# Kernel optimization log

Measured on AMD Instinct MI355X. Metric: run time of the kernel, lower is better.

Reference implementation:

```python
import jax, jax.numpy as jnp
import numpy as np
from jax import lax

B, T, D = 4, 4096, 1024
H, d = 4, 64
EPS = 1e-6

def pos_unit(x):
    # positive feature map (elu+1) normalized to unit L2 norm along feature dim
    p = jax.nn.elu(x) + 1.0
    return p / (jnp.linalg.norm(p, axis=-1, keepdims=True) + EPS)

def setup_inputs() -> dict:
    key = jax.random.key(0)
    ks = jax.random.split(key, 5)
    s_in = 1.0 / np.sqrt(D)
    s_hd = 1.0 / np.sqrt(H * d)
    return {
        "x": jax.random.normal(ks[0], (B, T, D), dtype=jnp.float32),
        "Wq": jax.random.normal(ks[1], (H * d, D), dtype=jnp.float32) * s_in,
        "Wk": jax.random.normal(ks[2], (H * d, D), dtype=jnp.float32) * s_in,
        "Wv": jax.random.normal(ks[3], (H * d, D), dtype=jnp.float32) * s_in,
        "Wo": jax.random.normal(ks[4], (D, H * d), dtype=jnp.float32) * s_hd,
    }

def reference(x, Wq, Wk, Wv, Wo):
    Bx, Tx, Dx = x.shape
    q = (x @ Wq.T).reshape(Bx, Tx, H, d)
    k = (x @ Wk.T).reshape(Bx, Tx, H, d)
    v = (x @ Wv.T).reshape(Bx, Tx, H, d)
    q = pos_unit(q)
    k = pos_unit(k)
    # time-major for scan: [T, B, H, d]
    qT = jnp.transpose(q, (1, 0, 2, 3))
    kT = jnp.transpose(k, (1, 0, 2, 3))
    vT = jnp.transpose(v, (1, 0, 2, 3))
    kv0 = jnp.zeros((Bx, H, d, d), dtype=x.dtype)  # [B,H,j,d]
    kc0 = jnp.zeros((Bx, H, d), dtype=x.dtype)

    def step(carry, inp):
        kv_cum, k_cum = carry
        qt, kt, vt = inp  # each [B,H,d]
        kv_cum = kv_cum + jnp.einsum('bhd,bhj->bhjd', kt, vt)
        k_cum = k_cum + kt
        num = jnp.einsum('bhd,bhjd->bhj', qt, kv_cum)
        den = jnp.einsum('bhd,bhd->bh', qt, k_cum)[..., None] + EPS
        return (kv_cum, k_cum), num / den

    (kv_f, kc_f), yT = lax.scan(step, (kv0, kc0), (qT, kT, vT))
    y = jnp.transpose(yT, (1, 0, 2, 3)).reshape(Bx, Tx, H * d)
    y = y @ Wo.T
    return y, kv_f, kc_f
```

## Files before the change

### kernel.cpp

```cpp
#include <hip/hip_runtime.h>
#include <hip/hip_bf16.h>
#include <math.h>

#define T_SEQ   4096
#define NB      4
#define NH      4
#define DH      64
#define DM      1024
#define MR      16384
#define NQKV    768
#define CH      64
#define NCH     64
#define SST     4160
#define BHN     16

typedef __attribute__((ext_vector_type(4))) float          f32x4;
typedef __attribute__((ext_vector_type(8))) short          s16x8;
typedef __attribute__((ext_vector_type(4))) unsigned short u16x4;

__device__ __forceinline__ float bf2f(unsigned short u) {
  union { unsigned int i; float f; } c; c.i = ((unsigned int)u) << 16; return c.f;
}
__device__ __forceinline__ unsigned short f2bf(float f) {
  union { float f; unsigned int i; } c; c.f = f;
  unsigned int i = c.i;
  return (unsigned short)((i + 0x7fffu + ((i >> 16) & 1u)) >> 16);
}
__device__ __forceinline__ s16x8 pack8(f32x4 lo, f32x4 hi) {
  s16x8 r;
  r[0] = (short)f2bf(lo.x); r[1] = (short)f2bf(lo.y);
  r[2] = (short)f2bf(lo.z); r[3] = (short)f2bf(lo.w);
  r[4] = (short)f2bf(hi.x); r[5] = (short)f2bf(hi.y);
  r[6] = (short)f2bf(hi.z); r[7] = (short)f2bf(hi.w);
  return r;
}

__global__ __launch_bounds__(256, 2) void gemm_qkv_kernel(
    const float* __restrict__ X,
    const float* __restrict__ Wq,
    const float* __restrict__ Wk,
    const float* __restrict__ Wv,
    unsigned short* __restrict__ C)
{
  constexpr int K = DM;
  constexpr int N = NQKV;
  __shared__ unsigned short sA[128 * 32];
  __shared__ unsigned short sB[128 * 32];

  const int tid  = threadIdx.x;
  const int wave = tid >> 6;
  const int lane = tid & 63;
  const int quad = lane >> 4;
  const int l16  = lane & 15;
  const int wm = (wave >> 1) * 64;
  const int wn = (wave & 1) * 64;

  const int row0 = blockIdx.x * 128;
  const int bn   = blockIdx.y;
  const float* Bt = (bn < 2) ? Wq : (bn < 4) ? Wk : Wv;
  const int brow0 = (bn & 1) * 128;

  const int srow = tid >> 2;
  const int scol = ((tid & 3) ^ (srow & 3)) * 8;
  const float* Ag = X  + (size_t)(row0  + srow) * K + scol;
  const float* Bg = Bt + (size_t)(brow0 + srow) * K + scol;
  unsigned short* sAp = sA + tid * 8;
  unsigned short* sBp = sB + tid * 8;

  const int ra = (quad ^ (l16 & 3)) * 8;

  f32x4 acc[4][4];
  #pragma unroll
  for (int i = 0; i < 4; i++)
    #pragma unroll
    for (int j = 0; j < 4; j++) acc[i][j] = (f32x4){0.f, 0.f, 0.f, 0.f};

  for (int kt = 0; kt < K; kt += 32) {
    const f32x4 a0l = *(const f32x4*)(Ag + kt);
    const f32x4 a0h = *(const f32x4*)(Ag + kt + 4);
    const f32x4 a1l = *(const f32x4*)(Ag + kt + (size_t)64 * K);
    const f32x4 a1h = *(const f32x4*)(Ag + kt + (size_t)64 * K + 4);
    const f32x4 b0l = *(const f32x4*)(Bg + kt);
    const f32x4 b0h = *(const f32x4*)(Bg + kt + 4);
    const f32x4 b1l = *(const f32x4*)(Bg + kt + (size_t)64 * K);
    const f32x4 b1h = *(const f32x4*)(Bg + kt + (size_t)64 * K + 4);
    __syncthreads();
    *(s16x8*)sAp          = pack8(a0l, a0h);
    *(s16x8*)(sAp + 2048) = pack8(a1l, a1h);
    *(s16x8*)sBp          = pack8(b0l, b0h);
    *(s16x8*)(sBp + 2048) = pack8(b1l, b1h);
    __syncthreads();
    s16x8 af[4], bw[4];
    #pragma unroll
    for (int i = 0; i < 4; i++)
      af[i] = *(const s16x8*)(sA + (wm + i * 16 + l16) * 32 + ra);
    #pragma unroll
    for (int j = 0; j < 4; j++)
      bw[j] = *(const s16x8*)(sB + (wn + j * 16 + l16) * 32 + ra);
    #pragma unroll
    for (int i = 0; i < 4; i++)
      #pragma unroll
      for (int j = 0; j < 4; j++)
        acc[i][j] = __builtin_amdgcn_mfma_f32_16x16x32_bf16(af[i], bw[j], acc[i][j], 0, 0, 0);
  }

  const int colb = bn * 128 + wn;
  #pragma unroll
  for (int i = 0; i < 4; i++) {
    const int r = row0 + wm + i * 16 + quad * 4;
    #pragma unroll
    for (int j = 0; j < 4; j++) {
      const int cc = colb + j * 16 + l16;
      #pragma unroll
      for (int g = 0; g < 4; g++)
        C[(size_t)(r + g) * N + cc] = f2bf(acc[i][j][g]);
    }
  }
}

__global__ __launch_bounds__(256, 2) void gemm_out_kernel(
    const unsigned short* __restrict__ Y,
    const float* __restrict__ Wo,
    float* __restrict__ Out)
{
  constexpr int K = 256;
  constexpr int N = DM;
  __shared__ unsigned short sA[128 * 32];
  __shared__ unsigned short sB[128 * 32];

  const int tid  = threadIdx.x;
  const int wave = tid >> 6;
  const int lane = tid & 63;
  const int quad = lane >> 4;
  const int l16  = lane & 15;
  const int wm = (wave >> 1) * 64;
  const int wn = (wave & 1) * 64;

  const int row0  = blockIdx.x * 128;
  const int bcol0 = blockIdx.y * 128;

  const int srow = tid >> 2;
  const int scol = ((tid & 3) ^ (srow & 3)) * 8;
  const unsigned short* Ag = Y  + (size_t)(row0  + srow) * K + scol;
  const float*          Bg = Wo + (size_t)(bcol0 + srow) * K + scol;
  unsigned short* sAp = sA + tid * 8;
  unsigned short* sBp = sB + tid * 8;

  const int ra = (quad ^ (l16 & 3)) * 8;

  f32x4 acc[4][4];
  #pragma unroll
  for (int i = 0; i < 4; i++)
    #pragma unroll
    for (int j = 0; j < 4; j++) acc[i][j] = (f32x4){0.f, 0.f, 0.f, 0.f};

  for (int kt = 0; kt < K; kt += 32) {
    const s16x8 a0 = *(const s16x8*)(Ag + kt);
    const s16x8 a1 = *(const s16x8*)(Ag + kt + (size_t)64 * K);
    const f32x4 b0l = *(const f32x4*)(Bg + kt);
    const f32x4 b0h = *(const f32x4*)(Bg + kt + 4);
    const f32x4 b1l = *(const f32x4*)(Bg + kt + (size_t)64 * K);
    const f32x4 b1h = *(const f32x4*)(Bg + kt + (size_t)64 * K + 4);
    __syncthreads();
    *(s16x8*)sAp          = a0;
    *(s16x8*)(sAp + 2048) = a1;
    *(s16x8*)sBp          = pack8(b0l, b0h);
    *(s16x8*)(sBp + 2048) = pack8(b1l, b1h);
    __syncthreads();
    s16x8 af[4], bw[4];
    #pragma unroll
    for (int i = 0; i < 4; i++)
      af[i] = *(const s16x8*)(sA + (wm + i * 16 + l16) * 32 + ra);
    #pragma unroll
    for (int j = 0; j < 4; j++)
      bw[j] = *(const s16x8*)(sB + (wn + j * 16 + l16) * 32 + ra);
    #pragma unroll
    for (int i = 0; i < 4; i++)
      #pragma unroll
      for (int j = 0; j < 4; j++)
        acc[i][j] = __builtin_amdgcn_mfma_f32_16x16x32_bf16(af[i], bw[j], acc[i][j], 0, 0, 0);
  }

  #pragma unroll
  for (int i = 0; i < 4; i++) {
    const int r = row0 + wm + i * 16 + quad * 4;
    #pragma unroll
    for (int j = 0; j < 4; j++) {
      const int cc = bcol0 + wn + j * 16 + l16;
      #pragma unroll
      for (int g = 0; g < 4; g++)
        Out[(size_t)(r + g) * N + cc] = acc[i][j][g];
    }
  }
}

__global__ __launch_bounds__(256) void chunk_sums_kernel(
    const unsigned short* __restrict__ qkv,
    float* __restrict__ cs)
{
  const int blk = blockIdx.x;
  const int bh = blk >> 6, c = blk & 63;
  const int b = bh >> 2, h = bh & 3;
  __shared__ float sK[CH * DH];
  __shared__ float sV[CH * DH];
  const int wave = threadIdx.x >> 6, lane = threadIdx.x & 63;
  const size_t rowbase = ((size_t)b * T_SEQ + (size_t)c * CH) * NQKV + h * DH;

  #pragma unroll 4
  for (int tt = 0; tt < 16; tt++) {
    const int t = tt * 4 + wave;
    const unsigned short* r = qkv + rowbase + (size_t)t * NQKV;
    const float kx = bf2f(r[256 + lane]);
    const float vx = bf2f(r[512 + lane]);
    float pk = kx > 0.f ? kx + 1.f : __expf(kx);
    float sk = pk * pk;
    #pragma unroll
    for (int o = 32; o > 0; o >>= 1) sk += __shfl_xor(sk, o, 64);
    sK[t * DH + lane] = pk / (sqrtf(sk) + 1e-6f);
    sV[t * DH + lane] = vx;
  }
  __syncthreads();

  const int dg = threadIdx.x >> 4;
  const int jg = threadIdx.x & 15;
  f32x4 a0 = (f32x4){0,0,0,0}, a1 = a0, a2 = a0, a3 = a0;
  for (int t = 0; t < CH; t++) {
    const f32x4 k4 = ((const f32x4*)sK)[t * 16 + dg];
    const f32x4 v4 = ((const f32x4*)sV)[t * 16 + jg];
    a0 += k4.x * v4; a1 += k4.y * v4; a2 += k4.z * v4; a3 += k4.w * v4;
  }
  float* o = cs + (size_t)blk * SST;
  ((f32x4*)(o + (dg * 4 + 0) * 64))[jg] = a0;
  ((f32x4*)(o + (dg * 4 + 1) * 64))[jg] = a1;
  ((f32x4*)(o + (dg * 4 + 2) * 64))[jg] = a2;
  ((f32x4*)(o + (dg * 4 + 3) * 64))[jg] = a3;
  if (threadIdx.x < 64) {
    float s = 0.f;
    for (int t = 0; t < CH; t++) s += sK[t * DH + threadIdx.x];
    o[4096 + threadIdx.x] = s;
  }
}

__global__ __launch_bounds__(256) void scan_kernel(
    float* __restrict__ cs, float* __restrict__ outTail)
{
  const int gid = blockIdx.x * 256 + threadIdx.x;
  const int bh = gid / SST;
  const int e  = gid - bh * SST;
  float run = 0.f;
  size_t idx = (size_t)bh * NCH * SST + e;
  for (int c = 0; c < NCH; c++, idx += SST) {
    const float v = cs[idx];
    cs[idx] = run;
    run += v;
  }
  if (e < 4096) {
    const int dd = e >> 6, j = e & 63;
    outTail[(size_t)bh * 4096 + j * 64 + dd] = run;
  } else {
    const int dd = e - 4096;
    outTail[BHN * 4096 + (size_t)bh * 64 + dd] = run;
  }
}

__global__ __launch_bounds__(256, 4) void chunk_out_kernel(
    const unsigned short* __restrict__ qkv,
    const float* __restrict__ st,
    unsigned short* __restrict__ yatt)
{
  const int blk = blockIdx.x;
  const int bh = blk >> 6;
  const int c  = blk & 63;
  const int b = bh >> 2, h = bh & 3;

  __shared__ __align__(16) unsigned short sQ [64 * 64];
  __shared__ __align__(16) unsigned short sKA[64 * 64];
  __shared__ __align__(16) unsigned short sVt[64 * 64];
  __shared__ __align__(16) unsigned short sSt[64 * 64];
  __shared__ float sKc[64];
  __shared__ float sDen[64];

  const int tid  = threadIdx.x;
  const int wave = tid >> 6, lane = tid & 63;
  const int quad = lane >> 4, l16 = lane & 15;
  const size_t rowbase = ((size_t)b * T_SEQ + (size_t)c * CH) * NQKV + h * DH;

  #pragma unroll 4
  for (int tt = 0; tt < 16; tt++) {
    const int t = tt * 4 + wave;
    const unsigned short* r = qkv + rowbase + (size_t)t * NQKV;
    const float qx = bf2f(r[lane]);
    const float kx = bf2f(r[256 + lane]);
    const unsigned short vu = r[512 + lane];
    float pq = qx > 0.f ? qx + 1.f : __expf(qx);
    float pk = kx > 0.f ? kx + 1.f : __expf(kx);
    float sq = pq * pq, sk = pk * pk;
    #pragma unroll
    for (int o = 32; o > 0; o >>= 1) {
      sq += __shfl_xor(sq, o, 64);
      sk += __shfl_xor(sk, o, 64);
    }
    const int sw = (t & 7) << 3;
    sQ [t * 64 + (lane ^ sw)] = f2bf(pq / (sqrtf(sq) + 1e-6f));
    sKA[t * 64 + (lane ^ sw)] = f2bf(pk / (sqrtf(sk) + 1e-6f));
    sVt[lane * 64 + (t ^ ((lane & 7) << 3))] = vu;
  }
  const float* stp = st + (size_t)blk * SST;
  for (int i = tid; i < 1024; i += 256) {
    const f32x4 s4 = ((const f32x4*)stp)[i];
    const int d = i >> 4, j0 = (i & 15) << 2;
    #pragma unroll
    for (int g = 0; g < 4; g++) {
      const int j = j0 + g;
      sSt[j * 64 + (d ^ ((j & 7) << 3))] = f2bf(s4[g]);
    }
  }
  if (tid < 64) sKc[tid] = stp[4096 + tid];
  __syncthreads();

  const int wr = (wave >> 1) * 32;
  const int wc = (wave & 1) * 32;

  f32x4 accA[2][2];
  #pragma unroll
  for (int i = 0; i < 2; i++)
    #pragma unroll
    for (int j = 0; j < 2; j++) accA[i][j] = (f32x4){0.f, 0.f, 0.f, 0.f};

  #pragma unroll
  for (int ks = 0; ks < 2; ks++) {
    const int grp = ks * 4 + quad;
    s16x8 aq[2], bk[2];
    #pragma unroll
    for (int i = 0; i < 2; i++) {
      const int rq = wr + i * 16 + l16;
      aq[i] = *(const s16x8*)(sQ + rq * 64 + ((grp ^ (rq & 7)) << 3));
    }
    #pragma unroll
    for (int j = 0; j < 2; j++) {
      const int rk = wc + j * 16 + l16;
      bk[j] = *(const s16x8*)(sKA + rk * 64 + ((grp ^ (rk & 7)) << 3));
    }
    #pragma unroll
    for (int i = 0; i < 2; i++)
      #pragma unroll
      for (int j = 0; j < 2; j++)
        accA[i][j] = __builtin_amdgcn_mfma_f32_16x16x32_bf16(aq[i], bk[j], accA[i][j], 0, 0, 0);
  }
  __syncthreads();

  #pragma unroll
  for (int i = 0; i < 2; i++)
    #pragma unroll
    for (int j = 0; j < 2; j++)
      #pragma unroll
      for (int g = 0; g < 4; g++) {
        const int t = wr + i * 16 + quad * 4 + g;
        const int s = wc + j * 16 + l16;
        const float av = (s <= t) ? accA[i][j][g] : 0.f;
        sKA[t * 64 + (s ^ ((t & 7) << 3))] = f2bf(av);
      }
  __syncthreads();

  {
    const int t = tid >> 2, p = tid & 3;
    const int sw = (t & 7) << 3;
    float s = 0.f;
    #pragma unroll
    for (int e = 0; e < 16; e++) {
      const int d = p * 16 + e;
      s += bf2f(sKA[t * 64 + d]);
      s += bf2f(sQ[t * 64 + (d ^ sw)]) * sKc[d];
    }
    s += __shfl_xor(s, 1, 64);
    s += __shfl_xor(s, 2, 64);
    if (p == 0) sDen[t] = s + 1e-6f;
  }
  __syncthreads();

  f32x4 acc[2][2];
  #pragma unroll
  for (int i = 0; i < 2; i++)
    #pragma unroll
    for (int j = 0; j < 2; j++) acc[i][j] = (f32x4){0.f, 0.f, 0.f, 0.f};

  #pragma unroll
  for (int ks = 0; ks < 2; ks++) {
    const int grp = ks * 4 + quad;
    s16x8 aq[2], bs[2];
    #pragma unroll
    for (int i = 0; i < 2; i++) {
      const int rq = wr + i * 16 + l16;
      aq[i] = *(const s16x8*)(sQ + rq * 64 + ((grp ^ (rq & 7)) << 3));
    }
    #pragma unroll
    for (int j = 0; j < 2; j++) {
      const int rj = wc + j * 16 + l16;
      bs[j] = *(const s16x8*)(sSt + rj * 64 + ((grp ^ (rj & 7)) << 3));
    }
    #pragma unroll
    for (int i = 0; i < 2; i++)
      #pragma unroll
      for (int j = 0; j < 2; j++)
        acc[i][j] = __builtin_amdgcn_mfma_f32_16x16x32_bf16(aq[i], bs[j], acc[i][j], 0, 0, 0);
  }
  #pragma unroll
  for (int ks = 0; ks < 2; ks++) {
    const int grp = ks * 4 + quad;
    s16x8 aa[2], bv[2];
    #pragma unroll
    for (int i = 0; i < 2; i++) {
      const int rt = wr + i * 16 + l16;
      aa[i] = *(const s16x8*)(sKA + rt * 64 + ((grp ^ (rt & 7)) << 3));
    }
    #pragma unroll
    for (int j = 0; j < 2; j++) {
      const int rj = wc + j * 16 + l16;
      bv[j] = *(const s16x8*)(sVt + rj * 64 + ((grp ^ (rj & 7)) << 3));
    }
    #pragma unroll
    for (int i = 0; i < 2; i++)
      #pragma unroll
      for (int j = 0; j < 2; j++)
        acc[i][j] = __builtin_amdgcn_mfma_f32_16x16x32_bf16(aa[i], bv[j], acc[i][j], 0, 0, 0);
  }

  #pragma unroll
  for (int i = 0; i < 2; i++)
    #pragma unroll
    for (int g = 0; g < 4; g++) {
      const int t = wr + i * 16 + quad * 4 + g;
      const float inv = 1.f / sDen[t];
      #pragma unroll
      for (int j = 0; j < 2; j++) {
        const int jj = wc + j * 16 + l16;
        const size_t o = ((size_t)b * T_SEQ + (size_t)c * CH + t) * 256 + h * 64 + jj;
        yatt[o] = f2bf(acc[i][j][g] * inv);
      }
    }
}

extern "C" void kernel_launch(void* const* d_in, const int* in_sizes, int n_in,
                              void* d_out, int out_size, void* d_ws, size_t ws_size,
                              hipStream_t stream) {
  const float* X  = (const float*)d_in[0];
  const float* Wq = (const float*)d_in[1];
  const float* Wk = (const float*)d_in[2];
  const float* Wv = (const float*)d_in[3];
  const float* Wo = (const float*)d_in[4];
  float* out = (float*)d_out;

  unsigned short* qkvb = (unsigned short*)d_out;
  float* outTail = out + 16777216;
  float*          cs   = (float*)d_ws;
  unsigned short* yatt = (unsigned short*)((char*)d_ws + 17039360ull);

  gemm_qkv_kernel  <<<dim3(128, 6), 256, 0, stream>>>(X, Wq, Wk, Wv, qkvb);
  chunk_sums_kernel<<<BHN * NCH,    256, 0, stream>>>(qkvb, cs);
  scan_kernel      <<<(BHN * SST) / 256, 256, 0, stream>>>(cs, outTail);
  chunk_out_kernel <<<BHN * NCH,    256, 0, stream>>>(qkvb, cs, yatt);
  gemm_out_kernel  <<<dim3(128, 8), 256, 0, stream>>>(yatt, Wo, out);
}
```

Baseline: 219.8 us.

## Pre-convert inputs to bf16 with direct global-to-LDS loads; MFMA chunk sums

Adds a separate kernel that converts X and the QKV weights to bf16 once, so the QKV GEMM can load bf16 tiles straight into LDS with global_load_lds and skip per-tile fp32 loads and register packing. The chunk-sum kernel now stores transposed, swizzled bf16 K and V in LDS and computes the K^T V outer-product sum with MFMA instead of scalar FMAs, taking the k-sum from per-wave partials. The cost is an extra launch plus a full read and write of X through scratch space in the output buffer, and lower precision for normalized K in the chunk sums.

```diff
diff --git a/kernel.cpp b/kernel.cpp
--- a/kernel.cpp
+++ b/kernel.cpp
@@ -34,18 +34,49 @@
   r[6] = (short)f2bf(hi.z); r[7] = (short)f2bf(hi.w);
   return r;
 }
+__device__ __forceinline__ void gl_lds16(const unsigned short* g, unsigned short* l) {
+  __builtin_amdgcn_global_load_lds(
+      (const __attribute__((address_space(1))) unsigned int*)g,
+      (__attribute__((address_space(3))) unsigned int*)l, 16, 0, 0);
+}
+
+__global__ __launch_bounds__(256) void convert_kernel(
+    const float* __restrict__ X,
+    const float* __restrict__ Wq, const float* __restrict__ Wk,
+    const float* __restrict__ Wv,
+    unsigned short* __restrict__ Xb, unsigned short* __restrict__ Wb)
+{
+  const long long NX = 16777216LL;
+  const long long NW = 786432LL;
+  const long long total = NX + NW;
+  const long long stride = (long long)gridDim.x * 256 * 8;
+  for (long long i = ((long long)blockIdx.x * 256 + threadIdx.x) * 8;
+       i < total; i += stride) {
+    const float* src;
+    unsigned short* dst;
+    if (i < NX) { src = X + i; dst = Xb + i; }
+    else {
+      const long long e = i - NX;
+      const int w = (int)(e >> 18);
+      const long long rr = e & 262143LL;
+      src = (w == 0 ? Wq : w == 1 ? Wk : Wv) + rr;
+      dst = Wb + e;
+    }
+    const f32x4 lo = *(const f32x4*)src;
+    const f32x4 hi = *(const f32x4*)(src + 4);
+    *(s16x8*)dst = pack8(lo, hi);
+  }
+}
 
 __global__ __launch_bounds__(256, 2) void gemm_qkv_kernel(
-    const float* __restrict__ X,
-    const float* __restrict__ Wq,
-    const float* __restrict__ Wk,
-    const float* __restrict__ Wv,
+    const unsigned short* __restrict__ Xb,
+    const unsigned short* __restrict__ Wb,
     unsigned short* __restrict__ C)
 {
   constexpr int K = DM;
   constexpr int N = NQKV;
-  __shared__ unsigned short sA[128 * 32];
-  __shared__ unsigned short sB[128 * 32];
+  __shared__ __align__(16) unsigned short sA[128 * 32];
+  __shared__ __align__(16) unsigned short sB[128 * 32];
 
   const int tid  = threadIdx.x;
   const int wave = tid >> 6;
@@ -57,13 +88,10 @@
 
   const int row0 = blockIdx.x * 128;
   const int bn   = blockIdx.y;
-  const float* Bt = (bn < 2) ? Wq : (bn < 4) ? Wk : Wv;
-  const int brow0 = (bn & 1) * 128;
-
   const int srow = tid >> 2;
   const int scol = ((tid & 3) ^ (srow & 3)) * 8;
-  const float* Ag = X  + (size_t)(row0  + srow) * K + scol;
-  const float* Bg = Bt + (size_t)(brow0 + srow) * K + scol;
+  const unsigned short* Ag = Xb + (size_t)(row0     + srow) * K + scol;
+  const unsigned short* Bg = Wb + (size_t)(bn * 128 + srow) * K + scol;
   unsigned short* sAp = sA + tid * 8;
   unsigned short* sBp = sB + tid * 8;
 
@@ -76,19 +104,11 @@
     for (int j = 0; j < 4; j++) acc[i][j] = (f32x4){0.f, 0.f, 0.f, 0.f};
 
   for (int kt = 0; kt < K; kt += 32) {
-    const f32x4 a0l = *(const f32x4*)(Ag + kt);
-    const f32x4 a0h = *(const f32x4*)(Ag + kt + 4);
-    const f32x4 a1l = *(const f32x4*)(Ag + kt + (size_t)64 * K);
-    const f32x4 a1h = *(const f32x4*)(Ag + kt + (size_t)64 * K + 4);
-    const f32x4 b0l = *(const f32x4*)(Bg + kt);
-    const f32x4 b0h = *(const f32x4*)(Bg + kt + 4);
-    const f32x4 b1l = *(const f32x4*)(Bg + kt + (size_t)64 * K);
-    const f32x4 b1h = *(const f32x4*)(Bg + kt + (size_t)64 * K + 4);
     __syncthreads();
-    *(s16x8*)sAp          = pack8(a0l, a0h);
-    *(s16x8*)(sAp + 2048) = pack8(a1l, a1h);
-    *(s16x8*)sBp          = pack8(b0l, b0h);
-    *(s16x8*)(sBp + 2048) = pack8(b1l, b1h);
+    gl_lds16(Ag + kt,                  sAp);
+    gl_lds16(Ag + kt + (size_t)64 * K, sAp + 2048);
+    gl_lds16(Bg + kt,                  sBp);
+    gl_lds16(Bg + kt + (size_t)64 * K, sBp + 2048);
     __syncthreads();
     s16x8 af[4], bw[4];
     #pragma unroll
@@ -201,44 +221,76 @@
   const int blk = blockIdx.x;
   const int bh = blk >> 6, c = blk & 63;
   const int b = bh >> 2, h = bh & 3;
-  __shared__ float sK[CH * DH];
-  __shared__ float sV[CH * DH];
+  __shared__ __align__(16) unsigned short sKt[64 * 64];
+  __shared__ __align__(16) unsigned short sVt[64 * 64];
+  __shared__ float sPart[4 * 64];
   const int wave = threadIdx.x >> 6, lane = threadIdx.x & 63;
+  const int quad = lane >> 4, l16 = lane & 15;
   const size_t rowbase = ((size_t)b * T_SEQ + (size_t)c * CH) * NQKV + h * DH;
 
+  float kacc = 0.f;
   #pragma unroll 4
   for (int tt = 0; tt < 16; tt++) {
     const int t = tt * 4 + wave;
     const unsigned short* r = qkv + rowbase + (size_t)t * NQKV;
     const float kx = bf2f(r[256 + lane]);
-    const float vx = bf2f(r[512 + lane]);
+    const unsigned short vu = r[512 + lane];
     float pk = kx > 0.f ? kx + 1.f : __expf(kx);
     float sk = pk * pk;
     #pragma unroll
     for (int o = 32; o > 0; o >>= 1) sk += __shfl_xor(sk, o, 64);
-    sK[t * DH + lane] = pk / (sqrtf(sk) + 1e-6f);
-    sV[t * DH + lane] = vx;
-  }
+    const float kn = pk / (sqrtf(sk) + 1e-6f);
+    kacc += kn;
+    const int sw = (lane & 7) << 3;
+    sKt[lane * 64 + (t ^ sw)] = f2bf(kn);
+    sVt[lane * 64 + (t ^ sw)] = vu;
+  }
+  sPart[wave * 64 + lane] = kacc;
   __syncthreads();
 
-  const int dg = threadIdx.x >> 4;
-  const int jg = threadIdx.x & 15;
-  f32x4 a0 = (f32x4){0,0,0,0}, a1 = a0, a2 = a0, a3 = a0;
-  for (int t = 0; t < CH; t++) {
-    const f32x4 k4 = ((const f32x4*)sK)[t * 16 + dg];
-    const f32x4 v4 = ((const f32x4*)sV)[t * 16 + jg];
-    a0 += k4.x * v4; a1 += k4.y * v4; a2 += k4.z * v4; a3 += k4.w * v4;
-  }
+  const int wr = (wave >> 1) * 32;
+  const int wc = (wave & 1) * 32;
+  f32x4 acc[2][2];
+  #pragma unroll
+  for (int i = 0; i < 2; i++)
+    #pragma unroll
+    for (int j = 0; j < 2; j++) acc[i][j] = (f32x4){0.f, 0.f, 0.f, 0.f};
+
+  #pragma unroll
+  for (int ks = 0; ks < 2; ks++) {
+    const int grp = ks * 4 + quad;
+    s16x8 ak[2], bv[2];
+    #pragma unroll
+    for (int i = 0; i < 2; i++) {
+      const int rk = wr + i * 16 + l16;
+      ak[i] = *(const s16x8*)(sKt + rk * 64 + ((grp ^ (rk & 7)) << 3));
+    }
+    #pragma unroll
+    for (int j = 0; j < 2; j++) {
+      const int rj = wc + j * 16 + l16;
+      bv[j] = *(const s16x8*)(sVt + rj * 64 + ((grp ^ (rj & 7)) << 3));
+    }
+    #pragma unroll
+    for (int i = 0; i < 2; i++)
+      #pragma unroll
+      for (int j = 0; j < 2; j++)
+        acc[i][j] = __builtin_amdgcn_mfma_f32_16x16x32_bf16(ak[i], bv[j], acc[i][j], 0, 0, 0);
+  }
+
   float* o = cs + (size_t)blk * SST;
-  ((f32x4*)(o + (dg * 4 + 0) * 64))[jg] = a0;
-  ((f32x4*)(o + (dg * 4 + 1) * 64))[jg] = a1;
-  ((f32x4*)(o + (dg * 4 + 2) * 64))[jg] = a2;
-  ((f32x4*)(o + (dg * 4 + 3) * 64))[jg] = a3;
-  if (threadIdx.x < 64) {
-    float s = 0.f;
-    for (int t = 0; t < CH; t++) s += sK[t * DH + threadIdx.x];
-    o[4096 + threadIdx.x] = s;
-  }
+  #pragma unroll
+  for (int i = 0; i < 2; i++)
+    #pragma unroll
+    for (int j = 0; j < 2; j++)
+      #pragma unroll
+      for (int g = 0; g < 4; g++) {
+        const int dd = wr + i * 16 + quad * 4 + g;
+        const int jj = wc + j * 16 + l16;
+        o[dd * 64 + jj] = acc[i][j][g];
+      }
+  if (threadIdx.x < 64)
+    o[4096 + threadIdx.x] = sPart[threadIdx.x] + sPart[64 + threadIdx.x]
+                          + sPart[128 + threadIdx.x] + sPart[192 + threadIdx.x];
 }
 
 __global__ __launch_bounds__(256) void scan_kernel(
@@ -451,11 +503,14 @@
   float* out = (float*)d_out;
 
   unsigned short* qkvb = (unsigned short*)d_out;
+  unsigned short* Xb   = (unsigned short*)((char*)d_out + 25165824ull);
+  unsigned short* Wb   = Xb + 16777216;
   float* outTail = out + 16777216;
   float*          cs   = (float*)d_ws;
   unsigned short* yatt = (unsigned short*)((char*)d_ws + 17039360ull);
 
-  gemm_qkv_kernel  <<<dim3(128, 6), 256, 0, stream>>>(X, Wq, Wk, Wv, qkvb);
+  convert_kernel   <<<4096,         256, 0, stream>>>(X, Wq, Wk, Wv, Xb, Wb);
+  gemm_qkv_kernel  <<<dim3(128, 6), 256, 0, stream>>>(Xb, Wb, qkvb);
   chunk_sums_kernel<<<BHN * NCH,    256, 0, stream>>>(qkvb, cs);
   scan_kernel      <<<(BHN * SST) / 256, 256, 0, stream>>>(cs, outTail);
   chunk_out_kernel <<<BHN * NCH,    256, 0, stream>>>(qkvb, cs, yatt);
```

Result: faster. 210.7 us (-4.2%).
